# Kernel tuning notes

Hardware: AMD Instinct MI355X
Metric: run time of the kernel (lower is better)

The kernel has to match this reference:

```python
import jax, jax.numpy as jnp
import numpy as np

B, C, H, W = 4, 512, 64, 64
NUM_HEADS = 4
NUM_GROUPS = 32
EPS = 1e-5


def setup_inputs() -> dict:
    key = jax.random.key(0)
    ks = jax.random.split(key, 7)
    x = jax.random.normal(ks[0], (B, C, H, W), dtype=jnp.float32)
    gn_gamma = jnp.ones((C,), dtype=jnp.float32)
    gn_beta = jnp.zeros((C,), dtype=jnp.float32)
    # Conv2d 1x1 weights stored as [out_ch, in_ch]
    qkv_w = jax.random.normal(ks[1], (3 * C, C), dtype=jnp.float32) * (C ** -0.5)
    qkv_b = jax.random.normal(ks[2], (3 * C,), dtype=jnp.float32) * 0.01
    out_w = jax.random.normal(ks[3], (C, C), dtype=jnp.float32) * (C ** -0.5)
    out_b = jax.random.normal(ks[4], (C,), dtype=jnp.float32) * 0.01
    return {"x": x, "gn_gamma": gn_gamma, "gn_beta": gn_beta,
            "qkv_w": qkv_w, "qkv_b": qkv_b, "out_w": out_w, "out_b": out_b}


def _group_norm(x, gamma, beta):
    b, c, h, w = x.shape
    xg = x.reshape(b, NUM_GROUPS, c // NUM_GROUPS, h, w)
    mean = xg.mean(axis=(2, 3, 4), keepdims=True)
    var = xg.var(axis=(2, 3, 4), keepdims=True)
    xg = (xg - mean) * jax.lax.rsqrt(var + EPS)
    x = xg.reshape(b, c, h, w)
    return x * gamma[None, :, None, None] + beta[None, :, None, None]


def reference(x, gn_gamma, gn_beta, qkv_w, qkv_b, out_w, out_b):
    residual = x
    b, c, h, w = x.shape
    hc = c // NUM_HEADS
    n = h * w
    xn = _group_norm(x, gn_gamma, gn_beta)
    # 1x1 conv == channel matmul: [B, 3C, H, W]
    qkv = jnp.einsum('oc,bchw->bohw', qkv_w, xn) + qkv_b[None, :, None, None]
    q, k, v = jnp.split(qkv, 3, axis=1)
    # [B, C, H, W] -> [B, heads, N, hc]
    def to_heads(t):
        return t.reshape(b, NUM_HEADS, hc, n).transpose(0, 1, 3, 2)
    q, k, v = to_heads(q), to_heads(k), to_heads(v)
    scale = hc ** -0.5
    attn = jnp.einsum('bhnd,bhmd->bhnm', q, k) * scale
    attn = jax.nn.softmax(attn, axis=-1)
    o = jnp.einsum('bhnm,bhmd->bhnd', attn, v)
    # back to [B, C, H, W]
    o = o.transpose(0, 1, 3, 2).reshape(b, c, h, w)
    o = o + residual
    out = jnp.einsum('oc,bchw->bohw', out_w, o) + out_b[None, :, None, None]
    return out
```

## Files before the change

### kernel.cpp

```cpp
#include <hip/hip_runtime.h>
#include <math.h>

constexpr int BB = 4, CH = 512, NN = 4096, NHEADS = 4, NGROUPS = 32, HCH = 128;
constexpr float EPS = 1e-5f;
constexpr float SCALE = 0.08838834764831845f;
constexpr float LOG2E = 1.4426950408889634f;
constexpr float QSCALE = SCALE * LOG2E;
constexpr float THR = 11.541560327111707f;

typedef short bf16x8 __attribute__((ext_vector_type(8)));
typedef float f32x4 __attribute__((ext_vector_type(4)));
typedef float f32x16 __attribute__((ext_vector_type(16)));

__device__ __forceinline__ float bf2f(unsigned short u) {
    unsigned int x = ((unsigned int)u) << 16;
    float f; __builtin_memcpy(&f, &x, 4); return f;
}
__device__ __forceinline__ unsigned short f2bf(float f) {
    unsigned int x; __builtin_memcpy(&x, &f, 4);
    x += 0x7fff + ((x >> 16) & 1);
    return (unsigned short)(x >> 16);
}
__device__ __forceinline__ unsigned int cvtpk(float lo, float hi) {
    unsigned int r;
    asm("v_cvt_pk_bf16_f32 %0, %1, %2" : "=v"(r) : "v"(lo), "v"(hi));
    return r;
}
__device__ __forceinline__ float fexp2(float x) {
    float r; asm("v_exp_f32 %0, %1" : "=v"(r) : "v"(x)); return r;
}

__device__ __forceinline__ void gld16(const void* g, void* l) {
    __builtin_amdgcn_global_load_lds(
        (const __attribute__((address_space(1))) void*)g,
        (__attribute__((address_space(3))) void*)l, 16, 0, 0);
}

__global__ __launch_bounds__(256) void prep_kernel(
    const float* __restrict__ qkv_w, const float* __restrict__ out_w,
    const float* __restrict__ x,
    unsigned short* __restrict__ wq_bf, unsigned short* __restrict__ wo_bf,
    float* __restrict__ stats)
{
    int bid = blockIdx.x;
    if (bid < 1024) {
        int i4 = bid * 256 + threadIdx.x;
        if (i4 < 196608) {
            float4 w = ((const float4*)qkv_w)[i4];
            int row = i4 >> 7;
            float sc = (row < 512) ? QSCALE : 1.0f;
            ushort4 o = { f2bf(w.x * sc), f2bf(w.y * sc), f2bf(w.z * sc), f2bf(w.w * sc) };
            *(ushort4*)&wq_bf[(size_t)i4 * 4] = o;
        } else {
            int j4 = i4 - 196608;
            float4 w = ((const float4*)out_w)[j4];
            ushort4 o = { f2bf(w.x), f2bf(w.y), f2bf(w.z), f2bf(w.w) };
            *(ushort4*)&wo_bf[(size_t)j4 * 4] = o;
        }
        return;
    }
    const int CPG = CH / NGROUPS;
    int gb = bid - 1024;
    int bg = gb >> 2, part = gb & 3;
    int b = bg / NGROUPS, g = bg % NGROUPS;
    const size_t base = ((size_t)b * CH + (size_t)g * CPG) * NN
                      + (size_t)part * (CPG * NN / 4);
    const int total4 = CPG * NN / 16;
    int tid = threadIdx.x;

    const float4* x4 = (const float4*)(x + base);
    float sum = 0.f, sumsq = 0.f;
    for (int i = tid; i < total4; i += 256) {
        float4 v = x4[i];
        sum   += v.x + v.y + v.z + v.w;
        sumsq += v.x*v.x + v.y*v.y + v.z*v.z + v.w*v.w;
    }
    for (int off = 32; off > 0; off >>= 1) {
        sum   += __shfl_down(sum, off);
        sumsq += __shfl_down(sumsq, off);
    }
    __shared__ float s_sum[4], s_sq[4];
    int wid = tid >> 6, lane = tid & 63;
    if (lane == 0) { s_sum[wid] = sum; s_sq[wid] = sumsq; }
    __syncthreads();
    if (tid == 0) {
        float ts = 0.f, tq = 0.f;
        for (int i = 0; i < 4; i++) { ts += s_sum[i]; tq += s_sq[i]; }
        atomicAdd(&stats[bg * 2 + 0], ts);
        atomicAdd(&stats[bg * 2 + 1], tq);
    }
}

__global__ __launch_bounds__(256) void t1_kernel(
    const float* __restrict__ x, const float2* __restrict__ stats,
    const float* __restrict__ gamma, const float* __restrict__ beta,
    unsigned short* __restrict__ xnT, unsigned short* __restrict__ xT)
{
    __shared__ alignas(16) short Tn[64 * 80];
    __shared__ alignas(16) short Tr[64 * 80];
    int n0 = blockIdx.x * 64, c0 = blockIdx.y * 64, b = blockIdx.z;
    int tid = threadIdx.x;
    const float inv = 1.0f / 65536.0f;

    #pragma unroll
    for (int i = 0; i < 4; ++i) {
        int idx = tid + i * 256; int cl = idx >> 4, nq = idx & 15;
        int c = c0 + cl;
        float2 st = stats[b * NGROUPS + (c >> 4)];
        float mean = st.x * inv;
        float var  = st.y * inv - mean * mean;
        float rstd = rsqrtf(var + EPS);
        float gm = gamma[c], bt = beta[c];
        float4 f = *(const float4*)&x[((size_t)(b * CH + c)) * NN + n0 + nq * 4];
        float e0 = f.x, e1 = f.y, e2 = f.z, e3 = f.w;
        Tr[(nq * 4 + 0) * 80 + cl] = (short)f2bf(e0);
        Tr[(nq * 4 + 1) * 80 + cl] = (short)f2bf(e1);
        Tr[(nq * 4 + 2) * 80 + cl] = (short)f2bf(e2);
        Tr[(nq * 4 + 3) * 80 + cl] = (short)f2bf(e3);
        Tn[(nq * 4 + 0) * 80 + cl] = (short)f2bf((e0 - mean) * rstd * gm + bt);
        Tn[(nq * 4 + 1) * 80 + cl] = (short)f2bf((e1 - mean) * rstd * gm + bt);
        Tn[(nq * 4 + 2) * 80 + cl] = (short)f2bf((e2 - mean) * rstd * gm + bt);
        Tn[(nq * 4 + 3) * 80 + cl] = (short)f2bf((e3 - mean) * rstd * gm + bt);
    }
    __syncthreads();
    #pragma unroll
    for (int i = 0; i < 2; ++i) {
        int idx = tid + i * 256; int n = idx >> 3, ck = idx & 7;
        size_t gidx = ((size_t)(b * NN + n0 + n)) * CH + c0 + ck * 8;
        *(uint4*)&xnT[gidx] = *(uint4*)&Tn[n * 80 + ck * 8];
        *(uint4*)&xT[gidx]  = *(uint4*)&Tr[n * 80 + ck * 8];
    }
}

template<int MODE>
__global__ __launch_bounds__(256) void gemm_kernel(
    const unsigned short* __restrict__ A,
    const unsigned short* __restrict__ Bt,
    const float* __restrict__ bias,
    unsigned short* __restrict__ qT, unsigned short* __restrict__ kT,
    unsigned short* __restrict__ v, float* __restrict__ out)
{
    __shared__ alignas(16) short smem[2][2][128 * 64];
    short* Es = (short*)smem;
    float* Ef = (float*)smem;

    constexpr int GY = (MODE == 0) ? 12 : 4;
    int lin = blockIdx.x + 32 * (blockIdx.y + GY * blockIdx.z);
    constexpr int CPX = 32 * GY * 4 / 8;
    int wg = (lin & 7) * CPX + (lin >> 3);
    const int n0 = (wg % 32) * 128;
    const int m0 = ((wg / 32) % GY) * 128;
    const int b  = wg / (32 * GY);

    const int tid = threadIdx.x;
    const int wid = tid >> 6, l = tid & 63, lr = l & 15, lk = l >> 4;
    const int wm = (wid & 1) * 64, wn = (wid >> 1) * 64;
    const unsigned short* Bb = Bt + (size_t)b * NN * CH;

    int rr[4], LL[4], ch[4];
    #pragma unroll
    for (int i = 0; i < 4; ++i) {
        ch[i] = (wid * 4 + i) * 1024;
        int li = ch[i] + l * 16;
        int r = li >> 7, s = (li >> 4) & 7;
        rr[i] = r; LL[i] = s ^ (r & 7);
    }

    #define GSTAGE(buf, k0) do {                                                   \
        _Pragma("unroll")                                                          \
        for (int i = 0; i < 4; ++i) {                                              \
            gld16(&A [((size_t)(m0 + rr[i])) * CH + (k0) + LL[i] * 8],             \
                  (char*)&smem[buf][0][0] + ch[i]);                                \
            gld16(&Bb[((size_t)(n0 + rr[i])) * CH + (k0) + LL[i] * 8],             \
                  (char*)&smem[buf][1][0] + ch[i]);                                \
        }                                                                          \
    } while (0)

    f32x4 acc[4][4];
    #pragma unroll
    for (int i = 0; i < 4; ++i)
        #pragma unroll
        for (int j = 0; j < 4; ++j) acc[i][j] = (f32x4){0.f, 0.f, 0.f, 0.f};

    GSTAGE(0, 0);
    __syncthreads();

    int cur = 0;
    for (int ks = 0; ks < 8; ++ks) {
        if (ks < 7) GSTAGE(cur ^ 1, (ks + 1) * 64);
        const char* As = (const char*)&smem[cur][0][0];
        const char* Bs = (const char*)&smem[cur][1][0];
        #pragma unroll
        for (int kh = 0; kh < 2; ++kh) {
            const int sw = ((kh * 4 + lk) ^ (lr & 7)) << 4;
            bf16x8 af[4], bfr[4];
            #pragma unroll
            for (int t = 0; t < 4; ++t) {
                af[t]  = *(const bf16x8*)(As + (wm + t * 16 + lr) * 128 + sw);
                bfr[t] = *(const bf16x8*)(Bs + (wn + t * 16 + lr) * 128 + sw);
            }
            #pragma unroll
            for (int mt = 0; mt < 4; ++mt)
                #pragma unroll
                for (int nt = 0; nt < 4; ++nt)
                    acc[mt][nt] = __builtin_amdgcn_mfma_f32_16x16x32_bf16(
                        af[mt], bfr[nt], acc[mt][nt], 0, 0, 0);
        }
        __syncthreads();
        cur ^= 1;
    }
    #undef GSTAGE

    if (MODE == 0) {
        const bool isV = (m0 >= 1024);
        #pragma unroll
        for (int mt = 0; mt < 4; ++mt) {
            int mbase = m0 + wm + mt * 16 + lk * 4;
            int ml = wm + mt * 16 + lk * 4;
            float bsc = (m0 < 512) ? QSCALE : 1.0f;
            #pragma unroll
            for (int nt = 0; nt < 4; ++nt) {
                int nl = wn + nt * 16 + lr;
                f32x4 vv = acc[mt][nt];
                if (!isV) {
                    ushort4 o;
                    o.x = f2bf(vv[0] + bias[mbase + 0] * bsc);
                    o.y = f2bf(vv[1] + bias[mbase + 1] * bsc);
                    o.z = f2bf(vv[2] + bias[mbase + 2] * bsc);
                    o.w = f2bf(vv[3] + bias[mbase + 3] * bsc);
                    *(ushort4*)&Es[nl * 132 + ml] = o;
                } else {
                    #pragma unroll
                    for (int j = 0; j < 4; ++j)
                        Es[(ml + j) * 132 + nl] = (short)f2bf(vv[j] + bias[mbase + j]);
                }
            }
        }
        __syncthreads();
        int r16 = tid >> 4, c16 = tid & 15;
        if (!isV) {
            unsigned short* dst;
            if (m0 < 512) dst = qT + (((size_t)(b * 4 + (m0 >> 7))) * NN + n0) * 128;
            else          dst = kT + (((size_t)(b * 4 + ((m0 - 512) >> 7))) * NN + n0) * 128;
            #pragma unroll
            for (int p = 0; p < 8; ++p) {
                int nl = p * 16 + r16;
                uint4 w = *(const uint4*)&Es[nl * 132 + c16 * 8];
                *(uint4*)&dst[(size_t)nl * 128 + c16 * 8] = w;
            }
        } else {
            unsigned short* dst = v + ((size_t)(b * 512 + (m0 - 1024)) * NN) + n0;
            #pragma unroll
            for (int p = 0; p < 8; ++p) {
                int ml = p * 16 + r16;
                uint4 w = *(const uint4*)&Es[ml * 132 + c16 * 8];
                *(uint4*)&dst[(size_t)ml * NN + c16 * 8] = w;
            }
        }
    } else {
        for (int half = 0; half < 2; ++half) {
            __syncthreads();
            if ((wn >> 6) == half) {
                #pragma unroll
                for (int mt = 0; mt < 4; ++mt) {
                    int ml = wm + mt * 16 + lk * 4;
                    int mbase = m0 + ml;
                    #pragma unroll
                    for (int nt = 0; nt < 4; ++nt) {
                        int nl = nt * 16 + lr;
                        f32x4 vv = acc[mt][nt];
                        #pragma unroll
                        for (int j = 0; j < 4; ++j)
                            Ef[(ml + j) * 66 + nl] = vv[j] + bias[mbase + j];
                    }
                }
            }
            __syncthreads();
            #pragma unroll
            for (int i = 0; i < 8; ++i) {
                int idx = tid + i * 256;
                int r = idx >> 4, c4 = idx & 15;
                float4 w = *(const float4*)&Ef[r * 66 + c4 * 4];
                *(float4*)&out[((size_t)(b * CH + m0 + r)) * NN + n0 + half * 64 + c4 * 4] = w;
            }
        }
    }
}

__global__ __launch_bounds__(256, 2) void attn_kernel(
    const unsigned short* __restrict__ qT,
    const unsigned short* __restrict__ kT,
    const unsigned short* __restrict__ vg,
    const unsigned short* __restrict__ xT,
    unsigned short* __restrict__ aoT)
{
    __shared__ alignas(16) short Ks[2][64 * 128];
    __shared__ alignas(16) short Vs[2][64 * 128];

    int lin_id = blockIdx.x + 32 * (blockIdx.y + 4 * blockIdx.z);
    int wg = (lin_id & 7) * 64 + (lin_id >> 3);
    const int n0 = (wg & 31) * 128;
    const int h  = (wg >> 5) & 3;
    const int b  = wg >> 7;

    const int bh = b * 4 + h;
    const int tid = threadIdx.x, wid = tid >> 6, l = tid & 63;
    const int lq = l & 31, hi = l >> 5;
    const int wq0 = wid * 32;
    const int swz4 = (l & 15) << 4;
    const unsigned short* Qg = qT + (size_t)bh * NN * 128;
    const unsigned short* Kg = kT + (size_t)bh * NN * 128;
    const unsigned short* Vg = vg + (size_t)bh * 128 * NN;

    int kr[4], kc[4], vdd[4], vcc[4], ch[4];
    #pragma unroll
    for (int i = 0; i < 4; ++i) {
        ch[i] = (wid * 4 + i) * 1024;
        int li = ch[i] + l * 16;
        int r = li >> 8, s = (li >> 4) & 15;
        int L = s ^ (r & 15);
        kr[i] = r; kc[i] = L;
        vdd[i] = r + 64 * (L >> 3);
        vcc[i] = L & 7;
    }

    #define STAGE(buf, m0k) do {                                                   \
        _Pragma("unroll")                                                          \
        for (int i = 0; i < 4; ++i) {                                              \
            gld16(&Kg[(size_t)((m0k) + kr[i]) * 128 + kc[i] * 8],                  \
                  (char*)&Ks[buf][0] + ch[i]);                                     \
            gld16(&Vg[(size_t)vdd[i] * NN + (m0k) + vcc[i] * 8],                   \
                  (char*)&Vs[buf][0] + ch[i]);                                     \
        }                                                                          \
    } while (0)

    STAGE(0, 0);

    bf16x8 qr[8];
    #pragma unroll
    for (int dk = 0; dk < 8; ++dk)
        qr[dk] = *(const bf16x8*)&Qg[((size_t)(n0 + wq0 + lq)) * 128 + dk * 16 + hi * 8];

    bf16x8 vone;
    #pragma unroll
    for (int j = 0; j < 8; ++j) vone[j] = (short)0x3F80;

    f32x16 ov[4], ovs;
    #pragma unroll
    for (int dt = 0; dt < 4; ++dt)
        #pragma unroll
        for (int r = 0; r < 16; ++r) ov[dt][r] = 0.f;
    #pragma unroll
    for (int r = 0; r < 16; ++r) ovs[r] = 0.f;
    float mrun = -1e30f;

    __syncthreads();

    int cur = 0;
    for (int t = 0; t < 64; ++t) {
        if (t < 63) STAGE(cur ^ 1, (t + 1) * 64);

        const char* Kc = (const char*)&Ks[cur][0];
        const char* Vc = (const char*)&Vs[cur][0];

        f32x16 s0, s1;
        #pragma unroll
        for (int r = 0; r < 16; ++r) { s0[r] = 0.f; s1[r] = 0.f; }
        __builtin_amdgcn_s_setprio(1);
        #pragma unroll
        for (int dk = 0; dk < 8; ++dk) {
            bf16x8 k0 = *(const bf16x8*)(Kc + (lq)      * 256 + ((dk * 32 + hi * 16) ^ swz4));
            bf16x8 k1 = *(const bf16x8*)(Kc + (32 + lq) * 256 + ((dk * 32 + hi * 16) ^ swz4));
            s0 = __builtin_amdgcn_mfma_f32_32x32x16_bf16(k0, qr[dk], s0, 0, 0, 0);
            s1 = __builtin_amdgcn_mfma_f32_32x32x16_bf16(k1, qr[dk], s1, 0, 0, 0);
        }
        __builtin_amdgcn_s_setprio(0);

        float m8[8];
        #pragma unroll
        for (int r = 0; r < 8; ++r)
            m8[r] = fmaxf(fmaxf(s0[r], s0[r + 8]), fmaxf(s1[r], s1[r + 8]));
        float t0 = fmaxf(fmaxf(m8[0], m8[1]), m8[2]);
        float t1_ = fmaxf(fmaxf(m8[3], m8[4]), m8[5]);
        float t2 = fmaxf(fmaxf(m8[6], m8[7]), t0);
        float pm = fmaxf(t1_, t2);
        pm = fmaxf(pm, __shfl_xor(pm, 32));

        int defer = (pm - mrun) <= THR;
        if (!__all(defer)) {
            float mnew = fmaxf(mrun, pm);
            float corr = fexp2(mrun - mnew);
            mrun = mnew;
            #pragma unroll
            for (int dt = 0; dt < 4; ++dt)
                #pragma unroll
                for (int r = 0; r < 16; ++r) ov[dt][r] *= corr;
            #pragma unroll
            for (int r = 0; r < 16; ++r) ovs[r] *= corr;
        }
        #pragma unroll
        for (int r = 0; r < 16; ++r) s0[r] = fexp2(s0[r] - mrun);
        #pragma unroll
        for (int r = 0; r < 16; ++r) s1[r] = fexp2(s1[r] - mrun);

        unsigned int u0[8], u1[8];
        #pragma unroll
        for (int m = 0; m < 8; ++m) {
            u0[m] = cvtpk(s0[2 * m], s0[2 * m + 1]);
            u1[m] = cvtpk(s1[2 * m], s1[2 * m + 1]);
        }
        bf16x8 pf[4];
        #pragma unroll
        for (int kt = 0; kt < 2; ++kt)
            #pragma unroll
            for (int hh = 0; hh < 2; ++hh) {
                const unsigned int* u = kt ? u1 : u0;
                unsigned int w0 = u[4*hh + 0], w2 = u[4*hh + 2];
                unsigned int w1 = u[4*hh + 1], w3 = u[4*hh + 3];
                asm("v_permlane32_swap_b32 %0, %1" : "+v"(w0), "+v"(w2));
                asm("v_permlane32_swap_b32 %0, %1" : "+v"(w1), "+v"(w3));
                unsigned int w[4] = { w0, w1, w2, w3 };
                bf16x8 p; __builtin_memcpy(&p, w, 16);
                pf[kt * 2 + hh] = p;
            }

        __builtin_amdgcn_s_setprio(1);
        #pragma unroll
        for (int dt = 0; dt < 4; ++dt)
            #pragma unroll
            for (int kt2 = 0; kt2 < 4; ++kt2) {
                bf16x8 vf = *(const bf16x8*)(Vc + ((dt & 1) * 32 + lq) * 256 +
                                             ((((dt >> 1) * 8 + kt2 * 2 + hi) << 4) ^ swz4));
                ov[dt] = __builtin_amdgcn_mfma_f32_32x32x16_bf16(vf, pf[kt2], ov[dt], 0, 0, 0);
            }
        #pragma unroll
        for (int kt2 = 0; kt2 < 4; ++kt2)
            ovs = __builtin_amdgcn_mfma_f32_32x32x16_bf16(vone, pf[kt2], ovs, 0, 0, 0);
        __builtin_amdgcn_s_setprio(0);

        __syncthreads();
        cur ^= 1;
    }
    #undef STAGE

    float linv = 1.0f / ovs[0];
    const int n = n0 + wq0 + lq;
    #pragma unroll
    for (int dt = 0; dt < 4; ++dt)
        #pragma unroll
        for (int m = 0; m < 4; ++m) {
            int d = dt * 32 + m * 8 + hi * 4;
            size_t gidx = ((size_t)(b * NN + n)) * CH + h * 128 + d;
            unsigned short xv[4];
            *(ushort4*)xv = *(const ushort4*)&xT[gidx];
            unsigned int w0 = cvtpk(ov[dt][4*m + 0] * linv + bf2f(xv[0]),
                                    ov[dt][4*m + 1] * linv + bf2f(xv[1]));
            unsigned int w1 = cvtpk(ov[dt][4*m + 2] * linv + bf2f(xv[2]),
                                    ov[dt][4*m + 3] * linv + bf2f(xv[3]));
            unsigned long long wv = (unsigned long long)w0 |
                                    ((unsigned long long)w1 << 32);
            *(unsigned long long*)&aoT[gidx] = wv;
        }
}

extern "C" void kernel_launch(void* const* d_in, const int* in_sizes, int n_in,
                              void* d_out, int out_size, void* d_ws, size_t ws_size,
                              hipStream_t stream) {
    const float* x      = (const float*)d_in[0];
    const float* gamma  = (const float*)d_in[1];
    const float* beta   = (const float*)d_in[2];
    const float* qkv_w  = (const float*)d_in[3];
    const float* qkv_b  = (const float*)d_in[4];
    const float* out_w  = (const float*)d_in[5];
    const float* out_b  = (const float*)d_in[6];
    float* out = (float*)d_out;

    char* ws = (char*)d_ws;
    const size_t SZ = (size_t)BB * CH * NN * 2;
    unsigned short* xnT   = (unsigned short*)(ws);
    unsigned short* xT    = (unsigned short*)(ws + SZ);
    unsigned short* qT    = (unsigned short*)(ws + 2 * SZ);
    unsigned short* kT    = (unsigned short*)(ws + 3 * SZ);
    unsigned short* vbuf  = (unsigned short*)(ws + 4 * SZ);
    unsigned short* aoT   = (unsigned short*)(ws + 5 * SZ);
    unsigned short* wq_bf = (unsigned short*)(ws + 6 * SZ);
    unsigned short* wo_bf = (unsigned short*)(ws + 6 * SZ + (size_t)1536 * 512 * 2);
    float* stats = (float*)(ws + 6 * SZ + (size_t)2048 * 512 * 2);

    hipMemsetAsync(stats, 0, 256 * sizeof(float), stream);
    prep_kernel<<<dim3(1536), 256, 0, stream>>>(qkv_w, out_w, x, wq_bf, wo_bf, stats);
    t1_kernel<<<dim3(NN / 64, CH / 64, BB), 256, 0, stream>>>(
        x, (const float2*)stats, gamma, beta, xnT, xT);
    gemm_kernel<0><<<dim3(NN / 128, 1536 / 128, BB), 256, 0, stream>>>(
        wq_bf, xnT, qkv_b, qT, kT, vbuf, nullptr);
    attn_kernel<<<dim3(NN / 128, NHEADS, BB), 256, 0, stream>>>(qT, kT, vbuf, xT, aoT);
    gemm_kernel<1><<<dim3(NN / 128, CH / 128, BB), 256, 0, stream>>>(
        wo_bf, aoT, out_b, nullptr, nullptr, nullptr, out);
}
```

Baseline: 260.4 us.

## Shrink attention blocks to 64 queries and drop LDS double-buffering

The attention kernel now uses 128-thread blocks covering 64 query rows each, with twice as many blocks, and a single K/V LDS buffer instead of two. Each iteration loads a tile, syncs, computes and syncs again, so global loads no longer overlap with the MFMA work. Halving LDS per block and threads per block is meant to raise occupancy and parallelism so other resident blocks can hide load latency. In exchange, K/V global traffic per query doubles and the in-block prefetch pipeline is lost.

Measured after the change: 283.5 us. 1.09x slower.

```diff
diff --git a/kernel.cpp b/kernel.cpp
--- a/kernel.cpp
+++ b/kernel.cpp
@@ -287,21 +287,21 @@
     }
 }
 
-__global__ __launch_bounds__(256, 2) void attn_kernel(
+__global__ __launch_bounds__(128, 2) void attn_kernel(
     const unsigned short* __restrict__ qT,
     const unsigned short* __restrict__ kT,
     const unsigned short* __restrict__ vg,
     const unsigned short* __restrict__ xT,
     unsigned short* __restrict__ aoT)
 {
-    __shared__ alignas(16) short Ks[2][64 * 128];
-    __shared__ alignas(16) short Vs[2][64 * 128];
-
-    int lin_id = blockIdx.x + 32 * (blockIdx.y + 4 * blockIdx.z);
-    int wg = (lin_id & 7) * 64 + (lin_id >> 3);
-    const int n0 = (wg & 31) * 128;
-    const int h  = (wg >> 5) & 3;
-    const int b  = wg >> 7;
+    __shared__ alignas(16) short Ks[64 * 128];
+    __shared__ alignas(16) short Vs[64 * 128];
+
+    int lin_id = blockIdx.x + 64 * (blockIdx.y + 4 * blockIdx.z);
+    int wg = (lin_id & 7) * 128 + (lin_id >> 3);
+    const int n0 = (wg & 63) * 64;
+    const int h  = (wg >> 6) & 3;
+    const int b  = wg >> 8;
 
     const int bh = b * 4 + h;
     const int tid = threadIdx.x, wid = tid >> 6, l = tid & 63;
@@ -312,30 +312,18 @@
     const unsigned short* Kg = kT + (size_t)bh * NN * 128;
     const unsigned short* Vg = vg + (size_t)bh * 128 * NN;
 
-    int kr[4], kc[4], vdd[4], vcc[4], ch[4];
-    #pragma unroll
-    for (int i = 0; i < 4; ++i) {
-        ch[i] = (wid * 4 + i) * 1024;
-        int li = ch[i] + l * 16;
-        int r = li >> 8, s = (li >> 4) & 15;
-        int L = s ^ (r & 15);
-        kr[i] = r; kc[i] = L;
-        vdd[i] = r + 64 * (L >> 3);
-        vcc[i] = L & 7;
-    }
-
-    #define STAGE(buf, m0k) do {                                                   \
+    #define STAGE(m0k) do {                                                        \
         _Pragma("unroll")                                                          \
-        for (int i = 0; i < 4; ++i) {                                              \
-            gld16(&Kg[(size_t)((m0k) + kr[i]) * 128 + kc[i] * 8],                  \
-                  (char*)&Ks[buf][0] + ch[i]);                                     \
-            gld16(&Vg[(size_t)vdd[i] * NN + (m0k) + vcc[i] * 8],                   \
-                  (char*)&Vs[buf][0] + ch[i]);                                     \
+        for (int i = 0; i < 8; ++i) {                                              \
+            int li = (wid * 8 + i) * 1024 + l * 16;                                \
+            int r = li >> 8, s = (li >> 4) & 15;                                   \
+            int L = s ^ (r & 15);                                                  \
+            gld16(&Kg[(size_t)((m0k) + r) * 128 + L * 8], (char*)Ks + li);         \
+            gld16(&Vg[(size_t)(r + 64 * (L >> 3)) * NN + (m0k) + (L & 7) * 8],     \
+                  (char*)Vs + li);                                                 \
         }                                                                          \
     } while (0)
 
-    STAGE(0, 0);
-
     bf16x8 qr[8];
     #pragma unroll
     for (int dk = 0; dk < 8; ++dk)
@@ -354,14 +342,9 @@
     for (int r = 0; r < 16; ++r) ovs[r] = 0.f;
     float mrun = -1e30f;
 
-    __syncthreads();
-
-    int cur = 0;
     for (int t = 0; t < 64; ++t) {
-        if (t < 63) STAGE(cur ^ 1, (t + 1) * 64);
-
-        const char* Kc = (const char*)&Ks[cur][0];
-        const char* Vc = (const char*)&Vs[cur][0];
+        STAGE(t * 64);
+        __syncthreads();
 
         f32x16 s0, s1;
         #pragma unroll
@@ -369,8 +352,8 @@
         __builtin_amdgcn_s_setprio(1);
         #pragma unroll
         for (int dk = 0; dk < 8; ++dk) {
-            bf16x8 k0 = *(const bf16x8*)(Kc + (lq)      * 256 + ((dk * 32 + hi * 16) ^ swz4));
-            bf16x8 k1 = *(const bf16x8*)(Kc + (32 + lq) * 256 + ((dk * 32 + hi * 16) ^ swz4));
+            bf16x8 k0 = *(const bf16x8*)((const char*)Ks + (lq)      * 256 + ((dk * 32 + hi * 16) ^ swz4));
+            bf16x8 k1 = *(const bf16x8*)((const char*)Ks + (32 + lq) * 256 + ((dk * 32 + hi * 16) ^ swz4));
             s0 = __builtin_amdgcn_mfma_f32_32x32x16_bf16(k0, qr[dk], s0, 0, 0, 0);
             s1 = __builtin_amdgcn_mfma_f32_32x32x16_bf16(k1, qr[dk], s1, 0, 0, 0);
         }
@@ -429,7 +412,7 @@
         for (int dt = 0; dt < 4; ++dt)
             #pragma unroll
             for (int kt2 = 0; kt2 < 4; ++kt2) {
-                bf16x8 vf = *(const bf16x8*)(Vc + ((dt & 1) * 32 + lq) * 256 +
+                bf16x8 vf = *(const bf16x8*)((const char*)Vs + ((dt & 1) * 32 + lq) * 256 +
                                              ((((dt >> 1) * 8 + kt2 * 2 + hi) << 4) ^ swz4));
                 ov[dt] = __builtin_amdgcn_mfma_f32_32x32x16_bf16(vf, pf[kt2], ov[dt], 0, 0, 0);
             }
@@ -439,7 +422,6 @@
         __builtin_amdgcn_s_setprio(0);
 
         __syncthreads();
-        cur ^= 1;
     }
     #undef STAGE
 
@@ -493,7 +475,7 @@
         x, (const float2*)stats, gamma, beta, xnT, xT);
     gemm_kernel<0><<<dim3(NN / 128, 1536 / 128, BB), 256, 0, stream>>>(
         wq_bf, xnT, qkv_b, qT, kT, vbuf, nullptr);
-    attn_kernel<<<dim3(NN / 128, NHEADS, BB), 256, 0, stream>>>(qT, kT, vbuf, xT, aoT);
+    attn_kernel<<<dim3(NN / 64, NHEADS, BB), 128, 0, stream>>>(qT, kT, vbuf, xT, aoT);
     gemm_kernel<1><<<dim3(NN / 128, CH / 128, BB), 256, 0, stream>>>(
         wo_bf, aoT, out_b, nullptr, nullptr, nullptr, out);
 }
```
